# Kernel optimization log

Hardware: AMD Instinct MI355X
Metric: run time of the kernel (lower is better)

Reference implementation:

```python
import jax, jax.numpy as jnp
import numpy as np
from jax import lax

DN = ('NCDHW', 'OIDHW', 'NCDHW')  # dimension numbers matching torch Conv3d (cross-correlation)


def setup_inputs() -> dict:
    key = jax.random.key(0)
    k0, k1, k2, k3 = jax.random.split(key, 4)
    B, P, C = 32, 2048, 512
    x = jax.random.normal(k0, (B, P, C), dtype=jnp.float32)
    w1 = jax.random.normal(k1, (1, 1, 1, 1, 1), dtype=jnp.float32)
    w2 = jax.random.normal(k2, (1, 1, 2, 2, 2), dtype=jnp.float32)
    w3 = jax.random.normal(k3, (1, 1, 3, 3, 3), dtype=jnp.float32)
    return {"x": x, "w1": w1, "w2": w2, "w3": w3}


def reference(x, w1, w2, w3):
    B, P, C = x.shape
    t = P // 16
    # [B,P,C] -> [B,C,t,4,4]
    xv = jnp.transpose(x, (0, 2, 1)).reshape(B, C, t, 4, 4)
    # x_shift: [B,t,C,4,4] -> [B*t, C, 4, 4]
    x_shift = jnp.transpose(xv, (0, 2, 1, 3, 4)).reshape(B * t, C, 4, 4)
    # channel mean -> [B,1,t,4,4]
    xm = jnp.mean(xv, axis=1, keepdims=True)
    # ST_1: 1x1x1 conv, no pad
    p1 = lax.conv_general_dilated(xm, w1, (1, 1, 1), 'VALID', dimension_numbers=DN)
    # ST_2: pad (left=1 on t,h,w), then 2x2x2 valid conv -> same shape
    xp = jnp.pad(xm, ((0, 0), (0, 0), (1, 0), (1, 0), (1, 0)))
    p2 = lax.conv_general_dilated(xp, w2, (1, 1, 1), 'VALID', dimension_numbers=DN)
    # ST_3: 3x3x3 conv with padding 1 -> same shape
    p3 = lax.conv_general_dilated(xm, w3, (1, 1, 1), [(1, 1), (1, 1), (1, 1)], dimension_numbers=DN)
    g = p1 + p2 + p3  # [B,1,t,4,4]
    # transpose(2,1) -> [B,t,1,4,4] -> [B*t,1,4,4]
    g = jnp.transpose(g, (0, 2, 1, 3, 4)).reshape(B * t, 1, 4, 4)
    out = x_shift * jax.nn.sigmoid(g)  # broadcast over C
    # back to [B,P,C]
    out = out.reshape(B, t, C, 4, 4)
    out = jnp.transpose(out, (0, 2, 1, 3, 4)).reshape(B, C, P)
    return jnp.transpose(out, (0, 2, 1))
```

## Files before the change

kernel.cpp:

```cpp
#include <hip/hip_runtime.h>
#include <math.h>

#define BB 32
#define PP 2048
#define CC 512
#define TT 128
#define NROWS (BB*PP)

__global__ __launch_bounds__(256) void row_mean_kernel(
        const float* __restrict__ x, float* __restrict__ mean) {
    int wave = threadIdx.x >> 6;
    int lane = threadIdx.x & 63;
    int row  = blockIdx.x * 4 + wave;
    const float4* xr = (const float4*)(x + (size_t)row * CC);
    float4 a = xr[lane];
    float4 b = xr[lane + 64];
    float s = (a.x + a.y) + (a.z + a.w) + (b.x + b.y) + (b.z + b.w);
    #pragma unroll
    for (int off = 32; off > 0; off >>= 1)
        s += __shfl_down(s, off, 64);
    if (lane == 0) mean[row] = s * (1.0f / 512.0f);
}

__global__ __launch_bounds__(256) void gate_kernel(
        const float* __restrict__ mean,
        const float* __restrict__ w1, const float* __restrict__ w2,
        const float* __restrict__ w3, float* __restrict__ gate) {
    int r = blockIdx.x * blockDim.x + threadIdx.x;
    if (r >= NROWS) return;
    int b = r >> 11;
    int p = r & 2047;
    int t = p >> 4;
    int h = (p >> 2) & 3;
    int w = p & 3;
    const float* mb = mean + ((size_t)b << 11);
    float g = 0.0f;
    #pragma unroll
    for (int i = 0; i < 3; ++i) {
        int tt = t + i - 1;
        if (tt < 0 || tt >= TT) continue;
        #pragma unroll
        for (int j = 0; j < 3; ++j) {
            int hh = h + j - 1;
            if (hh < 0 || hh >= 4) continue;
            #pragma unroll
            for (int k = 0; k < 3; ++k) {
                int ww = w + k - 1;
                if (ww < 0 || ww >= 4) continue;
                float wt = w3[i * 9 + j * 3 + k];
                if (i < 2 && j < 2 && k < 2) wt += w2[i * 4 + j * 2 + k];
                if (i == 1 && j == 1 && k == 1) wt += w1[0];
                g += wt * mb[tt * 16 + hh * 4 + ww];
            }
        }
    }
    gate[r] = 1.0f / (1.0f + __expf(-g));
}

__global__ __launch_bounds__(256) void scale_kernel(
        const float* __restrict__ x, const float* __restrict__ gate,
        float* __restrict__ out) {
    size_t q = (size_t)blockIdx.x * blockDim.x + threadIdx.x;
    int r = (int)(q >> 7);
    float s = gate[r];
    float4 v = ((const float4*)x)[q];
    v.x *= s; v.y *= s; v.z *= s; v.w *= s;
    ((float4*)out)[q] = v;
}

extern "C" void kernel_launch(void* const* d_in, const int* in_sizes, int n_in,
                              void* d_out, int out_size, void* d_ws, size_t ws_size,
                              hipStream_t stream) {
    const float* x  = (const float*)d_in[0];
    const float* w1 = (const float*)d_in[1];
    const float* w2 = (const float*)d_in[2];
    const float* w3 = (const float*)d_in[3];
    float* out  = (float*)d_out;
    float* mean = (float*)d_ws;
    float* gate = mean + NROWS;

    row_mean_kernel<<<NROWS / 4, 256, 0, stream>>>(x, mean);
    gate_kernel<<<NROWS / 256, 256, 0, stream>>>(mean, w1, w2, w3, gate);
    scale_kernel<<<(NROWS * (CC / 4)) / 256, 256, 0, stream>>>(x, gate, out);
}
```

Before: 249.8 us.

## Fuse mean, gate conv and scaling into one kernel per time tile

Replaces the three kernels (row mean, gate conv, scale) with a single kernel. Each block owns one (batch, t) tile of 16 rows, holds the tile in registers, computes its channel means, and recomputes the halo means of the neighbouring t planes from global memory. It then evaluates the 3x3x3 gate in shared memory and writes the scaled output. This removes the second full read of x and the intermediate mean and gate buffers, at the cost of reading the halo rows twice more. Block indices are also swizzled to spread neighbouring tiles across XCDs.

```diff
diff --git a/kernel.cpp b/kernel.cpp
--- a/kernel.cpp
+++ b/kernel.cpp
@@ -7,65 +7,109 @@
 #define TT 128
 #define NROWS (BB*PP)
 
-__global__ __launch_bounds__(256) void row_mean_kernel(
-        const float* __restrict__ x, float* __restrict__ mean) {
-    int wave = threadIdx.x >> 6;
-    int lane = threadIdx.x & 63;
-    int row  = blockIdx.x * 4 + wave;
-    const float4* xr = (const float4*)(x + (size_t)row * CC);
-    float4 a = xr[lane];
-    float4 b = xr[lane + 64];
-    float s = (a.x + a.y) + (a.z + a.w) + (b.x + b.y) + (b.z + b.w);
+__global__ __launch_bounds__(256) void fused_kernel(
+        const float* __restrict__ x,
+        const float* __restrict__ w1, const float* __restrict__ w2,
+        const float* __restrict__ w3, float* __restrict__ out) {
+    __shared__ float smean[3][16];
+    __shared__ float spart[4][8];
+    __shared__ float sgate[16];
+
+    int bid = blockIdx.x;
+    int wg  = ((bid & 7) << 9) | (bid >> 3);
+    int b = wg >> 7;
+    int t = wg & 127;
+
+    int tid  = threadIdx.x;
+    int wave = tid >> 6;
+    int lane = tid & 63;
+
+    size_t tile_f4 = ((size_t)(b * TT + t) * 16) * (CC / 4);
+    const float4* xt = (const float4*)x + tile_f4;
+    float4*       ot = (float4*)out     + tile_f4;
+
+    float4 v[8];
     #pragma unroll
-    for (int off = 32; off > 0; off >>= 1)
-        s += __shfl_down(s, off, 64);
-    if (lane == 0) mean[row] = s * (1.0f / 512.0f);
-}
+    for (int j = 0; j < 8; ++j) v[j] = xt[tid + 256 * j];
 
-__global__ __launch_bounds__(256) void gate_kernel(
-        const float* __restrict__ mean,
-        const float* __restrict__ w1, const float* __restrict__ w2,
-        const float* __restrict__ w3, float* __restrict__ gate) {
-    int r = blockIdx.x * blockDim.x + threadIdx.x;
-    if (r >= NROWS) return;
-    int b = r >> 11;
-    int p = r & 2047;
-    int t = p >> 4;
-    int h = (p >> 2) & 3;
-    int w = p & 3;
-    const float* mb = mean + ((size_t)b << 11);
-    float g = 0.0f;
+    int hr    = tid >> 3;
+    int hu    = tid & 7;
+    int plane = hr >> 4;
+    int rloc  = hr & 15;
+    int ht    = t + (plane ? 1 : -1);
+    bool hvalid = (ht >= 0) && (ht < TT);
+    float hsum = 0.0f;
+    if (hvalid) {
+        const float4* hrow = (const float4*)x +
+            ((size_t)(b * TT + ht) * 16 + rloc) * (CC / 4);
+        #pragma unroll
+        for (int j = 0; j < 16; ++j) {
+            float4 hv = hrow[hu + 8 * j];
+            hsum += (hv.x + hv.y) + (hv.z + hv.w);
+        }
+    }
+
+    if (tid < 48) ((float*)smean)[tid] = 0.0f;
+
     #pragma unroll
-    for (int i = 0; i < 3; ++i) {
-        int tt = t + i - 1;
-        if (tt < 0 || tt >= TT) continue;
+    for (int j = 0; j < 8; ++j) {
+        float s = (v[j].x + v[j].y) + (v[j].z + v[j].w);
         #pragma unroll
-        for (int j = 0; j < 3; ++j) {
-            int hh = h + j - 1;
-            if (hh < 0 || hh >= 4) continue;
+        for (int off = 32; off > 0; off >>= 1)
+            s += __shfl_down(s, off, 64);
+        if (lane == 0) spart[wave][j] = s;
+    }
+
+    hsum += __shfl_down(hsum, 4, 64);
+    hsum += __shfl_down(hsum, 2, 64);
+    hsum += __shfl_down(hsum, 1, 64);
+
+    __syncthreads();
+
+    if (hu == 0 && hvalid)
+        smean[plane ? 2 : 0][rloc] = hsum * (1.0f / 512.0f);
+    if (tid < 16) {
+        int jj = tid >> 1;
+        float s = (tid & 1) ? (spart[2][jj] + spart[3][jj])
+                            : (spart[0][jj] + spart[1][jj]);
+        smean[1][tid] = s * (1.0f / 512.0f);
+    }
+
+    __syncthreads();
+
+    if (tid < 16) {
+        int h  = tid >> 2;
+        int w_ = tid & 3;
+        float g = 0.0f;
+        #pragma unroll
+        for (int i = 0; i < 3; ++i) {
             #pragma unroll
-            for (int k = 0; k < 3; ++k) {
-                int ww = w + k - 1;
-                if (ww < 0 || ww >= 4) continue;
-                float wt = w3[i * 9 + j * 3 + k];
-                if (i < 2 && j < 2 && k < 2) wt += w2[i * 4 + j * 2 + k];
-                if (i == 1 && j == 1 && k == 1) wt += w1[0];
-                g += wt * mb[tt * 16 + hh * 4 + ww];
+            for (int j = 0; j < 3; ++j) {
+                int hh = h + j - 1;
+                if (hh < 0 || hh > 3) continue;
+                #pragma unroll
+                for (int k = 0; k < 3; ++k) {
+                    int ww = w_ + k - 1;
+                    if (ww < 0 || ww > 3) continue;
+                    float wt = w3[i * 9 + j * 3 + k];
+                    if (i < 2 && j < 2 && k < 2) wt += w2[i * 4 + j * 2 + k];
+                    if (i == 1 && j == 1 && k == 1) wt += w1[0];
+                    g += wt * smean[i][hh * 4 + ww];
+                }
             }
         }
+        sgate[tid] = 1.0f / (1.0f + __expf(-g));
     }
-    gate[r] = 1.0f / (1.0f + __expf(-g));
-}
 
-__global__ __launch_bounds__(256) void scale_kernel(
-        const float* __restrict__ x, const float* __restrict__ gate,
-        float* __restrict__ out) {
-    size_t q = (size_t)blockIdx.x * blockDim.x + threadIdx.x;
-    int r = (int)(q >> 7);
-    float s = gate[r];
-    float4 v = ((const float4*)x)[q];
-    v.x *= s; v.y *= s; v.z *= s; v.w *= s;
-    ((float4*)out)[q] = v;
+    __syncthreads();
+
+    #pragma unroll
+    for (int j = 0; j < 8; ++j) {
+        float s = sgate[(tid + 256 * j) >> 7];
+        float4 o = v[j];
+        o.x *= s; o.y *= s; o.z *= s; o.w *= s;
+        ot[tid + 256 * j] = o;
+    }
 }
 
 extern "C" void kernel_launch(void* const* d_in, const int* in_sizes, int n_in,
@@ -75,11 +119,7 @@
     const float* w1 = (const float*)d_in[1];
     const float* w2 = (const float*)d_in[2];
     const float* w3 = (const float*)d_in[3];
-    float* out  = (float*)d_out;
-    float* mean = (float*)d_ws;
-    float* gate = mean + NROWS;
+    float* out = (float*)d_out;
 
-    row_mean_kernel<<<NROWS / 4, 256, 0, stream>>>(x, mean);
-    gate_kernel<<<NROWS / 256, 256, 0, stream>>>(mean, w1, w2, w3, gate);
-    scale_kernel<<<(NROWS * (CC / 4)) / 256, 256, 0, stream>>>(x, gate, out);
+    fused_kernel<<<BB * TT, 256, 0, stream>>>(x, w1, w2, w3, out);
 }
```

After: 243.3 us. 2.6% less time.
